# Kernel optimization log

Hardware: AMD Instinct MI355X
Metric: run time of the kernel (lower is better)

Reference implementation:

```python
import jax, jax.numpy as jnp
import numpy as np

DIM = 1024
NH = 16
HD = DIM // NH  # 64
WINDOW = 8      # window_size; flash window=(WINDOW-1, -1) with causal=True
EPS_NORM = 1e-6


def _rmsnorm(h, w):
    # RMSNorm over last dim (full model dim, applied before head split)
    return h * jax.lax.rsqrt(jnp.mean(h * h, axis=-1, keepdims=True) + EPS_NORM) * w


def _rope(h, cos, sin):
    # h: [bv, L, NH, HD]; cos/sin: [L, HD//2]; torch view-as-complex pairs adjacent elems
    hr = h[..., 0::2]
    hi = h[..., 1::2]
    c = cos[None, :, None, :]
    s = sin[None, :, None, :]
    out_r = hr * c - hi * s
    out_i = hr * s + hi * c
    return jnp.stack([out_r, out_i], axis=-1).reshape(h.shape)


def setup_inputs() -> dict:
    key = jax.random.key(0)
    ks = jax.random.split(key, 8)
    bv, f, nlt = 1, 16, 1472
    b = bv * f
    L = f * nlt
    wscale = DIM ** -0.5
    x = jax.random.normal(ks[0], (b, nlt, DIM), jnp.float32)
    # standard RoPE tables, base 10000, d//2 frequencies
    pos = jnp.arange(L, dtype=jnp.float32)[:, None]
    inv_freq = 1.0 / (10000.0 ** (jnp.arange(HD // 2, dtype=jnp.float32) / (HD // 2)))
    ang = pos * inv_freq[None, :]
    inp = {
        'x': x,
        'freqs_cos': jnp.cos(ang),
        'freqs_sin': jnp.sin(ang),
        'q_w': jax.random.normal(ks[1], (DIM, DIM), jnp.float32) * wscale,
        'q_b': jnp.zeros((DIM,), jnp.float32),
        'k_w': jax.random.normal(ks[2], (DIM, DIM), jnp.float32) * wscale,
        'k_b': jnp.zeros((DIM,), jnp.float32),
        'v_w': jax.random.normal(ks[3], (DIM, DIM), jnp.float32) * wscale,
        'v_b': jnp.zeros((DIM,), jnp.float32),
        'o_w': jax.random.normal(ks[4], (DIM, DIM), jnp.float32) * wscale,
        'o_b': jnp.zeros((DIM,), jnp.float32),
        'norm_q_w': jnp.ones((DIM,), jnp.float32),
        'norm_k_w': jnp.ones((DIM,), jnp.float32),
        'bv': 1,
        'f': 16,
        'nlt': 1472,
    }
    return inp


def reference(x, freqs_cos, freqs_sin, q_w, q_b, k_w, k_b, v_w, v_b, o_w, o_b,
              norm_q_w, norm_k_w, bv, f, nlt):
    b, s = x.shape[:2]  # b = bv*f, s = nlt
    q = _rmsnorm(x @ q_w.T + q_b, norm_q_w)
    k = _rmsnorm(x @ k_w.T + k_b, norm_k_w)
    v = (x @ v_w.T + v_b).reshape(bv, f, s, NH, HD)
    # RoPE over flattened (frame, token) positions
    q4 = q.reshape(bv, f * s, NH, HD)
    k4 = k.reshape(bv, f * s, NH, HD)
    qr = _rope(q4, freqs_cos, freqs_sin)
    kr = _rope(k4, freqs_cos, freqs_sin)
    # temporal layout: [bv*nlt, f, NH, HD] (attend over frames per latent token)
    qr = qr.reshape(bv, f, s, NH, HD).transpose(0, 2, 1, 3, 4).reshape(bv * s, f, NH, HD)
    kr = kr.reshape(bv, f, s, NH, HD).transpose(0, 2, 1, 3, 4).reshape(bv * s, f, NH, HD)
    vr = v.transpose(0, 2, 1, 3, 4).reshape(bv * s, f, NH, HD)
    # causal sliding-window mask over frames: j <= i and i - j < WINDOW
    fi = jnp.arange(f)
    mask = (fi[None, :] <= fi[:, None]) & (fi[:, None] - fi[None, :] < WINDOW)  # [f, f]
    scores = jnp.einsum('bqhd,bkhd->bhqk', qr, kr) / np.float32(np.sqrt(HD))
    scores = jnp.where(mask[None, None], scores, jnp.float32(-1e30))
    attn = jax.nn.softmax(scores, axis=-1)
    o = jnp.einsum('bhqk,bkhd->bqhd', attn, vr)  # [bv*nlt, f, NH, HD]
    o = o.reshape(bv, s, f, NH, HD).transpose(0, 2, 1, 3, 4).reshape(bv * f, s, DIM)
    return o @ o_w.T + o_b
```

## Files before the change

### kernel.cpp

```cpp
#include <hip/hip_runtime.h>
#include <hip/hip_bf16.h>
#include <math.h>

typedef __bf16 bf16;
typedef bf16 bf16x8 __attribute__((ext_vector_type(8)));
typedef bf16 bf16x4 __attribute__((ext_vector_type(4)));
typedef float f32x4 __attribute__((ext_vector_type(4)));

#define NFRM 16
#define SEQ  1472
#define TOK  (NFRM * SEQ)
#define DIM_ 1024
#define NH_  16
#define HD_  64
#define KROW 1032


__device__ __forceinline__ void load_lds_16B(const void* g, void* l) {
  __builtin_amdgcn_global_load_lds(
      (const __attribute__((address_space(1))) unsigned int*)g,
      (__attribute__((address_space(3))) unsigned int*)l,
      16, 0, 0);
}

__global__ __launch_bounds__(256) void cvt_bf16(const float* __restrict__ s,
                                                bf16* __restrict__ d, int n) {
  size_t i = ((size_t)blockIdx.x * 256 + threadIdx.x) * 8;
  if (i >= (size_t)n) return;
  f32x4 a = *(const f32x4*)(s + i);
  f32x4 b = *(const f32x4*)(s + i + 4);
  bf16x8 o;
  o[0] = (bf16)a[0]; o[1] = (bf16)a[1]; o[2] = (bf16)a[2]; o[3] = (bf16)a[3];
  o[4] = (bf16)b[0]; o[5] = (bf16)b[1]; o[6] = (bf16)b[2]; o[7] = (bf16)b[3];
  *(bf16x8*)(d + i) = o;
}

__global__ __launch_bounds__(256) void cvt_w4(
    const float* __restrict__ w0, const float* __restrict__ w1,
    const float* __restrict__ w2, const float* __restrict__ w3,
    bf16* __restrict__ d0, bf16* __restrict__ d1,
    bf16* __restrict__ d2, bf16* __restrict__ d3) {
  const int z = blockIdx.y;
  const float* s = (z == 0) ? w0 : (z == 1) ? w1 : (z == 2) ? w2 : w3;
  bf16* d       = (z == 0) ? d0 : (z == 1) ? d1 : (z == 2) ? d2 : d3;
  size_t i = ((size_t)blockIdx.x * 256 + threadIdx.x) * 8;
  f32x4 a = *(const f32x4*)(s + i);
  f32x4 b = *(const f32x4*)(s + i + 4);
  bf16x8 o;
  o[0] = (bf16)a[0]; o[1] = (bf16)a[1]; o[2] = (bf16)a[2]; o[3] = (bf16)a[3];
  o[4] = (bf16)b[0]; o[5] = (bf16)b[1]; o[6] = (bf16)b[2]; o[7] = (bf16)b[3];
  *(bf16x8*)(d + i) = o;
}

template <typename OutT, int AMAP>
__device__ __forceinline__ void gemm256_body(const bf16* __restrict__ A,
                                             const bf16* __restrict__ B,
                                             const float* __restrict__ bias,
                                             OutT* __restrict__ C,
                                             bf16* lds) {
  const int tid  = threadIdx.x;
  const int w    = tid >> 6;
  const int lane = tid & 63;
  const int am0  = blockIdx.x * 256;
  const int bn0  = blockIdx.y * 256;

  const int rstep = w * 8 + (lane >> 3);
  const int jsrc  = ((lane & 7) ^ ((lane >> 3) & 7)) * 8;
  const int arb[4] = {0, 128, 64, 192};
  const bf16* srcp[8];
  int dstoff[8];
#pragma unroll
  for (int s = 0; s < 4; ++s) {
    srcp[s]   = B + (size_t)(bn0 + s * 64 + rstep) * DIM_ + jsrc;
    dstoff[s] = 32768 + s * 8192 + w * 1024;
    int R = am0 + arb[s] + rstep;
    size_t ar;
    if (AMAP == 1)      ar = (size_t)(R & 15) * SEQ + (R >> 4);
    else if (AMAP == 2) { unsigned f = (unsigned)R / SEQ;
                          ar = (size_t)(R - (int)f * SEQ) * 16 + f; }
    else                 ar = (size_t)R;
    srcp[4 + s]   = A + ar * DIM_ + jsrc;
    dstoff[4 + s] = arb[s] * 128 + w * 1024;
  }

  const int wr   = w >> 2;
  const int wc   = w & 3;
  const int frow = lane & 15;
  const int g    = lane >> 4;
  const int sw   = (frow & 7) << 4;
  const int e0   = (g * 16) ^ sw;
  const int e1   = (g * 16 + 64) ^ sw;
  const int aA   = (wr * 128 + frow) * 128;
  const int bB   = 32768 + (wc * 64 + frow) * 128;

  f32x4 acc[8][4];
#pragma unroll
  for (int i = 0; i < 8; ++i)
#pragma unroll
    for (int j = 0; j < 4; ++j) {
      f32x4 z = {0.f, 0.f, 0.f, 0.f};
      acc[i][j] = z;
    }

  char* ldsc = (char*)lds;

#pragma unroll
  for (int s = 0; s < 8; ++s) load_lds_16B(srcp[s], ldsc + dstoff[s]);

#pragma unroll 1
  for (int it = 0; it < 8; ++it) {
#pragma unroll
    for (int half = 0; half < 2; ++half) {
      const int kt   = it * 2 + half;
      const int cur  = half ? 65536 : 0;
      const int nxt  = half ? 0 : 65536;
      const int kpre = (kt < 15) ? (kt + 1) * 64 : 15 * 64;

      asm volatile("s_waitcnt vmcnt(2)" ::: "memory");
      asm volatile("s_barrier" ::: "memory");
#pragma unroll
      for (int s = 0; s < 4; ++s)
        load_lds_16B(srcp[s] + kpre, ldsc + nxt + dstoff[s]);

      bf16x8 bfv[4][2];
#pragma unroll
      for (int j = 0; j < 4; ++j) {
        bfv[j][0] = *(const bf16x8*)(ldsc + cur + bB + j * 2048 + e0);
        bfv[j][1] = *(const bf16x8*)(ldsc + cur + bB + j * 2048 + e1);
      }

#pragma unroll
      for (int p = 0; p < 4; ++p) {
        if (p == 1) {
          load_lds_16B(srcp[4] + kpre, ldsc + nxt + dstoff[4]);
          load_lds_16B(srcp[5] + kpre, ldsc + nxt + dstoff[5]);
        }
        if (p == 2) {
          asm volatile("s_waitcnt vmcnt(6)" ::: "memory");
          asm volatile("s_barrier" ::: "memory");
          load_lds_16B(srcp[6] + kpre, ldsc + nxt + dstoff[6]);
          load_lds_16B(srcp[7] + kpre, ldsc + nxt + dstoff[7]);
        }
        bf16x8 af[2][2];
#pragma unroll
        for (int ii = 0; ii < 2; ++ii) {
          const int i = p * 2 + ii;
          af[ii][0] = *(const bf16x8*)(ldsc + cur + aA + i * 2048 + e0);
          af[ii][1] = *(const bf16x8*)(ldsc + cur + aA + i * 2048 + e1);
        }
        __builtin_amdgcn_s_setprio(1);
#pragma unroll
        for (int ii = 0; ii < 2; ++ii) {
          const int i = p * 2 + ii;
#pragma unroll
          for (int j = 0; j < 4; ++j) {
            acc[i][j] = __builtin_amdgcn_mfma_f32_16x16x32_bf16(
                af[ii][0], bfv[j][0], acc[i][j], 0, 0, 0);
            acc[i][j] = __builtin_amdgcn_mfma_f32_16x16x32_bf16(
                af[ii][1], bfv[j][1], acc[i][j], 0, 0, 0);
          }
        }
        __builtin_amdgcn_s_setprio(0);
      }
    }
  }

  const int cl = lane & 15;
  const int rq = g * 4;
#pragma unroll
  for (int j = 0; j < 4; ++j) {
    const int nc   = bn0 + wc * 64 + j * 16 + cl;
    const float bb = bias[nc];
#pragma unroll
    for (int i = 0; i < 8; ++i) {
#pragma unroll
      for (int r = 0; r < 4; ++r) {
        const size_t mr = (size_t)am0 + wr * 128 + i * 16 + rq + r;
        C[mr * DIM_ + nc] = (OutT)(acc[i][j][r] + bb);
      }
    }
  }
}

__global__ __launch_bounds__(512, 2) void gemm_qkv(
    const bf16* __restrict__ A,
    const bf16* __restrict__ Bq, const bf16* __restrict__ Bk,
    const bf16* __restrict__ Bv,
    const float* __restrict__ bq, const float* __restrict__ bk,
    const float* __restrict__ bv,
    bf16* __restrict__ Cq, bf16* __restrict__ Ck, bf16* __restrict__ Cv) {
  __shared__ __align__(16) bf16 lds[65536];
  const int z = blockIdx.z;
  const bf16* B    = (z == 0) ? Bq : (z == 1) ? Bk : Bv;
  const float* bia = (z == 0) ? bq : (z == 1) ? bk : bv;
  bf16* C          = (z == 0) ? Cq : (z == 1) ? Ck : Cv;
  gemm256_body<bf16, 1>(A, B, bia, C, lds);
}

__global__ __launch_bounds__(512, 2) void gemm_out(
    const bf16* __restrict__ A, const bf16* __restrict__ B,
    const float* __restrict__ bias, float* __restrict__ C) {
  __shared__ __align__(16) bf16 lds[65536];
  gemm256_body<float, 2>(A, B, bias, C, lds);
}

__global__ __launch_bounds__(256) void norm_rope(
    bf16* __restrict__ q, bf16* __restrict__ k,
    const float* __restrict__ nqw, const float* __restrict__ nkw,
    const float* __restrict__ fcos, const float* __restrict__ fsin) {
  const int lane = threadIdx.x & 63, wave = threadIdx.x >> 6;
  const size_t row  = (size_t)blockIdx.x * 4 + wave;
  const size_t base = row * DIM_;
  const size_t pos  = (row & 15) * (size_t)SEQ + (row >> 4);
  const int e0 = lane * 16;
  const int j0 = (lane & 3) * 8;

  float cs[8], sn[8];
#pragma unroll
  for (int i = 0; i < 8; ++i) {
    cs[i] = fcos[pos * 32 + j0 + i];
    sn[i] = fsin[pos * 32 + j0 + i];
  }

  bf16x8 qa = *(const bf16x8*)(q + base + e0);
  bf16x8 qb = *(const bf16x8*)(q + base + e0 + 8);
  bf16x8 ka = *(const bf16x8*)(k + base + e0);
  bf16x8 kb = *(const bf16x8*)(k + base + e0 + 8);

  float xq[16], xk[16];
#pragma unroll
  for (int i = 0; i < 8; ++i) {
    xq[i] = (float)qa[i]; xq[8 + i] = (float)qb[i];
    xk[i] = (float)ka[i]; xk[8 + i] = (float)kb[i];
  }
  float sq = 0.f, sk = 0.f;
#pragma unroll
  for (int i = 0; i < 16; ++i) { sq += xq[i] * xq[i]; sk += xk[i] * xk[i]; }
#pragma unroll
  for (int off = 32; off > 0; off >>= 1) {
    sq += __shfl_xor(sq, off);
    sk += __shfl_xor(sk, off);
  }
  const float rq = rsqrtf(sq * (1.0f / 1024.0f) + 1e-6f);
  const float rk = rsqrtf(sk * (1.0f / 1024.0f) + 1e-6f);
#pragma unroll
  for (int i = 0; i < 16; ++i) {
    xq[i] *= rq * nqw[e0 + i];
    xk[i] *= rk * nkw[e0 + i];
  }
  bf16x8 oa, ob, oc, od;
#pragma unroll
  for (int p = 0; p < 8; ++p) {
    const float c = cs[p], s = sn[p];
    const float q0 = xq[2 * p], q1 = xq[2 * p + 1];
    const float k0 = xk[2 * p], k1 = xk[2 * p + 1];
    const float qr = q0 * c - q1 * s, qi = q0 * s + q1 * c;
    const float kr = k0 * c - k1 * s, ki = k0 * s + k1 * c;
    if (p < 4) { oa[2 * p] = (bf16)qr; oa[2 * p + 1] = (bf16)qi;
                 oc[2 * p] = (bf16)kr; oc[2 * p + 1] = (bf16)ki; }
    else       { ob[2 * p - 8] = (bf16)qr; ob[2 * p - 7] = (bf16)qi;
                 od[2 * p - 8] = (bf16)kr; od[2 * p - 7] = (bf16)ki; }
  }
  *(bf16x8*)(q + base + e0)     = oa;
  *(bf16x8*)(q + base + e0 + 8) = ob;
  *(bf16x8*)(k + base + e0)     = oc;
  *(bf16x8*)(k + base + e0 + 8) = od;
}

__global__ __launch_bounds__(512, 4) void attn_win(
    const bf16* __restrict__ q, const bf16* __restrict__ k,
    const bf16* __restrict__ v, bf16* __restrict__ o) {
  __shared__ __align__(16) bf16 ks[16 * KROW];
  __shared__ __align__(16) bf16 vs[16 * KROW];
  __shared__ __align__(16) bf16 ps[16 * 256];
  const int t    = blockIdx.x;
  const int tid  = threadIdx.x;
  const int wave = tid >> 6, lane = tid & 63;
  const size_t tb = (size_t)t * (16 * DIM_);

#pragma unroll
  for (int i = 0; i < 4; ++i) {
    const int j = wave * 4 + i;
    const int r = j >> 1, half = j & 1;
    const size_t g = tb + (size_t)r * DIM_ + half * 512 + lane * 8;
    load_lds_16B(k + g, ks + r * KROW + half * 512);
    load_lds_16B(v + g, vs + r * KROW + half * 512);
  }
  __syncthreads();

  const int fl  = lane & 15;
  const int kq  = (lane >> 4) * 8;
#pragma unroll
  for (int hh = 0; hh < 2; ++hh) {
    const int h = wave * 2 + hh;
    const size_t qg = tb + (size_t)fl * DIM_ + h * HD_ + kq;
    bf16x8 aq0 = *(const bf16x8*)(q + qg);
    bf16x8 aq1 = *(const bf16x8*)(q + qg + 32);
    const int ko = fl * KROW + h * HD_ + kq;
    bf16x8 bk0 = *(const bf16x8*)(ks + ko);
    bf16x8 bk1 = *(const bf16x8*)(ks + ko + 32);
    f32x4 sc = {0.f, 0.f, 0.f, 0.f};
    sc = __builtin_amdgcn_mfma_f32_16x16x32_bf16(aq0, bk0, sc, 0, 0, 0);
    sc = __builtin_amdgcn_mfma_f32_16x16x32_bf16(aq1, bk1, sc, 0, 0, 0);
#pragma unroll
    for (int r = 0; r < 4; ++r) {
      const int row = (lane >> 4) * 4 + r;
      const bool valid = (fl <= row) && (row - fl < 8);
      float s = valid ? sc[r] * 0.125f : -1e30f;
      float m = s;
#pragma unroll
      for (int off = 8; off > 0; off >>= 1) m = fmaxf(m, __shfl_xor(m, off));
      const float e = __expf(s - m);
      float su = e;
#pragma unroll
      for (int off = 8; off > 0; off >>= 1) su += __shfl_xor(su, off);
      ps[h * 256 + row * 16 + fl] = (bf16)(e / su);
    }
  }
  __syncthreads();

  const int h3 = tid >> 5;
  const int dc = (tid >> 2) & 7;
  const int fg = tid & 3;
  bf16x8 pr[8];
#pragma unroll
  for (int i = 0; i < 4; ++i) {
    pr[2 * i]     = *(const bf16x8*)(ps + h3 * 256 + (fg * 4 + i) * 16);
    pr[2 * i + 1] = *(const bf16x8*)(ps + h3 * 256 + (fg * 4 + i) * 16 + 8);
  }
  float acc[4][8];
#pragma unroll
  for (int i = 0; i < 4; ++i)
#pragma unroll
    for (int d = 0; d < 8; ++d) acc[i][d] = 0.f;

  const bf16* vb = vs + h3 * HD_ + dc * 8;
#pragma unroll
  for (int fk2 = 0; fk2 < 16; ++fk2) {
    bf16x8 vv8 = *(const bf16x8*)(vb + fk2 * KROW);
    float vf[8];
#pragma unroll
    for (int d = 0; d < 8; ++d) vf[d] = (float)vv8[d];
#pragma unroll
    for (int i = 0; i < 4; ++i) {
      const float pp = (float)((fk2 < 8) ? pr[2 * i][fk2] : pr[2 * i + 1][fk2 - 8]);
#pragma unroll
      for (int d = 0; d < 8; ++d) acc[i][d] += pp * vf[d];
    }
  }
#pragma unroll
  for (int i = 0; i < 4; ++i) {
    bf16x8 ov;
#pragma unroll
    for (int d = 0; d < 8; ++d) ov[d] = (bf16)acc[i][d];
    *(bf16x8*)(o + tb + (size_t)(fg * 4 + i) * DIM_ + h3 * HD_ + dc * 8) = ov;
  }
}

extern "C" void kernel_launch(void* const* d_in, const int* in_sizes, int n_in,
                              void* d_out, int out_size, void* d_ws,
                              size_t ws_size, hipStream_t stream) {
  const float* x    = (const float*)d_in[0];
  const float* fcos = (const float*)d_in[1];
  const float* fsin = (const float*)d_in[2];
  const float* q_w  = (const float*)d_in[3];
  const float* q_b  = (const float*)d_in[4];
  const float* k_w  = (const float*)d_in[5];
  const float* k_b  = (const float*)d_in[6];
  const float* v_w  = (const float*)d_in[7];
  const float* v_b  = (const float*)d_in[8];
  const float* o_w  = (const float*)d_in[9];
  const float* o_b  = (const float*)d_in[10];
  const float* nqw  = (const float*)d_in[11];
  const float* nkw  = (const float*)d_in[12];
  float* out = (float*)d_out;

  char* ws = (char*)d_ws;
  const size_t SZ  = (size_t)TOK * DIM_ * 2;
  const size_t WSZ = (size_t)DIM_ * DIM_ * 2;
  bf16* xb = (bf16*)(ws);
  bf16* wq = (bf16*)(ws + SZ);
  bf16* wk = (bf16*)(ws + SZ + WSZ);
  bf16* wv = (bf16*)(ws + SZ + 2 * WSZ);
  bf16* wo = (bf16*)(ws + SZ + 3 * WSZ);
  bf16* qq = (bf16*)(ws + SZ + 4 * WSZ);
  bf16* kk = (bf16*)(ws + SZ + 4 * WSZ + SZ);
  bf16* vv = (bf16*)(ws + SZ + 4 * WSZ + 2 * SZ);
  bf16* om = xb;

  const int NTOT = TOK * DIM_;
  const int NW   = DIM_ * DIM_;

  cvt_bf16<<<NTOT / 2048, 256, 0, stream>>>(x, xb, NTOT);
  cvt_w4<<<dim3(NW / 2048, 4), 256, 0, stream>>>(q_w, k_w, v_w, o_w,
                                                 wq, wk, wv, wo);

  dim3 gq(TOK / 256, DIM_ / 256, 3);
  gemm_qkv<<<gq, 512, 0, stream>>>(xb, wq, wk, wv, q_b, k_b, v_b, qq, kk, vv);

  norm_rope<<<TOK / 4, 256, 0, stream>>>(qq, kk, nqw, nkw, fcos, fsin);

  attn_win<<<SEQ, 512, 0, stream>>>(qq, kk, vv, om);

  gemm_out<<<dim3(TOK / 256, DIM_ / 256), 512, 0, stream>>>(om, wo, o_b, out);
}
```

Baseline: 551.5 us.

## Permute rows during input conversion and remap GEMM tiles for L2 locality

The fp32-to-bf16 conversion of x now writes rows already in token-major (t*16+f) order, so the QKV GEMM reads A contiguously instead of gathering scattered rows. The inverse permutation moves from the A-load path of the output GEMM to its store path, so attention output is read contiguously and fp32 results are scattered on write. Both GEMMs also remap the flat block index with an XCD-aware swizzle, so tiles sharing A and B rows land on the same die for better L2 reuse. The cost is strided, uncoalesced row writes in the conversion kernel and the output-GEMM epilogue.

Result: faster. 536.5 us (-2.7%).

```diff
diff --git a/kernel.cpp b/kernel.cpp
--- a/kernel.cpp
+++ b/kernel.cpp
@@ -27,12 +27,17 @@
                                                 bf16* __restrict__ d, int n) {
   size_t i = ((size_t)blockIdx.x * 256 + threadIdx.x) * 8;
   if (i >= (size_t)n) return;
+  const int r   = (int)(i >> 10);
+  const int col = (int)(i & 1023);
+  const int f   = r / SEQ;
+  const int t   = r - f * SEQ;
+  const size_t o = ((size_t)(t * 16 + f) << 10) + col;
   f32x4 a = *(const f32x4*)(s + i);
   f32x4 b = *(const f32x4*)(s + i + 4);
-  bf16x8 o;
-  o[0] = (bf16)a[0]; o[1] = (bf16)a[1]; o[2] = (bf16)a[2]; o[3] = (bf16)a[3];
-  o[4] = (bf16)b[0]; o[5] = (bf16)b[1]; o[6] = (bf16)b[2]; o[7] = (bf16)b[3];
-  *(bf16x8*)(d + i) = o;
+  bf16x8 v;
+  v[0] = (bf16)a[0]; v[1] = (bf16)a[1]; v[2] = (bf16)a[2]; v[3] = (bf16)a[3];
+  v[4] = (bf16)b[0]; v[5] = (bf16)b[1]; v[6] = (bf16)b[2]; v[7] = (bf16)b[3];
+  *(bf16x8*)(d + o) = v;
 }
 
 __global__ __launch_bounds__(256) void cvt_w4(
@@ -52,17 +57,23 @@
   *(bf16x8*)(d + i) = o;
 }
 
-template <typename OutT, int AMAP>
+__device__ __forceinline__ void swz368(int h, int& bx, int& by) {
+  const int s = (h & 7) * 46 + (h >> 3);
+  bx = s >> 2;
+  by = s & 3;
+}
+
+template <typename OutT, int OMAP>
 __device__ __forceinline__ void gemm256_body(const bf16* __restrict__ A,
                                              const bf16* __restrict__ B,
                                              const float* __restrict__ bias,
                                              OutT* __restrict__ C,
-                                             bf16* lds) {
+                                             bf16* lds, int bx, int by) {
   const int tid  = threadIdx.x;
   const int w    = tid >> 6;
   const int lane = tid & 63;
-  const int am0  = blockIdx.x * 256;
-  const int bn0  = blockIdx.y * 256;
+  const int am0  = bx * 256;
+  const int bn0  = by * 256;
 
   const int rstep = w * 8 + (lane >> 3);
   const int jsrc  = ((lane & 7) ^ ((lane >> 3) & 7)) * 8;
@@ -73,13 +84,7 @@
   for (int s = 0; s < 4; ++s) {
     srcp[s]   = B + (size_t)(bn0 + s * 64 + rstep) * DIM_ + jsrc;
     dstoff[s] = 32768 + s * 8192 + w * 1024;
-    int R = am0 + arb[s] + rstep;
-    size_t ar;
-    if (AMAP == 1)      ar = (size_t)(R & 15) * SEQ + (R >> 4);
-    else if (AMAP == 2) { unsigned f = (unsigned)R / SEQ;
-                          ar = (size_t)(R - (int)f * SEQ) * 16 + f; }
-    else                 ar = (size_t)R;
-    srcp[4 + s]   = A + ar * DIM_ + jsrc;
+    srcp[4 + s]   = A + (size_t)(am0 + arb[s] + rstep) * DIM_ + jsrc;
     dstoff[4 + s] = arb[s] * 128 + w * 1024;
   }
 
@@ -175,7 +180,10 @@
     for (int i = 0; i < 8; ++i) {
 #pragma unroll
       for (int r = 0; r < 4; ++r) {
-        const size_t mr = (size_t)am0 + wr * 128 + i * 16 + rq + r;
+        const int rowp = am0 + wr * 128 + i * 16 + rq + r;
+        const size_t mr = (OMAP == 1)
+            ? ((size_t)(rowp & 15) * SEQ + (rowp >> 4))
+            : (size_t)rowp;
         C[mr * DIM_ + nc] = (OutT)(acc[i][j][r] + bb);
       }
     }
@@ -194,14 +202,18 @@
   const bf16* B    = (z == 0) ? Bq : (z == 1) ? Bk : Bv;
   const float* bia = (z == 0) ? bq : (z == 1) ? bk : bv;
   bf16* C          = (z == 0) ? Cq : (z == 1) ? Ck : Cv;
-  gemm256_body<bf16, 1>(A, B, bia, C, lds);
+  int bx, by;
+  swz368(blockIdx.y * 92 + blockIdx.x, bx, by);
+  gemm256_body<bf16, 0>(A, B, bia, C, lds, bx, by);
 }
 
 __global__ __launch_bounds__(512, 2) void gemm_out(
     const bf16* __restrict__ A, const bf16* __restrict__ B,
     const float* __restrict__ bias, float* __restrict__ C) {
   __shared__ __align__(16) bf16 lds[65536];
-  gemm256_body<float, 2>(A, B, bias, C, lds);
+  int bx, by;
+  swz368(blockIdx.y * 92 + blockIdx.x, bx, by);
+  gemm256_body<float, 1>(A, B, bias, C, lds, bx, by);
 }
 
 __global__ __launch_bounds__(256) void norm_rope(
```
